# Kernel tuning notes

Measured on AMD Instinct MI355X. Metric: run time of the kernel, lower is better.

The kernel has to match this reference:

```python
import jax, jax.numpy as jnp
import numpy as np

L, B, F, D = 12, 2048, 6144, 768

def setup_inputs() -> dict:
    key = jax.random.key(0)
    k1, k2, k3 = jax.random.split(key, 3)
    acts = jax.random.normal(k1, (L, B, F), dtype=jnp.float32)
    # decoder weights for target layer: stacked per source layer, [L, F, D]
    W = jax.random.normal(k2, (L, F, D), dtype=jnp.float32) * 0.02
    bias = jax.random.normal(k3, (L, D), dtype=jnp.float32) * 0.01
    return {"acts": acts, "W": W, "bias": bias, "layer_idx": 11}

def reference(acts, W, bias, layer_idx):
    # decode(): sum over src_layer <= layer_idx of Linear(a[src], W[src->tgt], b[src->tgt])
    n = layer_idx + 1  # static Python int -> static slice
    a = acts[:n]       # [n, B, F]
    w = W[:n]          # [n, F, D]
    b = bias[:n]       # [n, D]
    # fused accumulation of all per-source-layer GEMMs
    recon = jnp.einsum('lbf,lfd->bd', a, w) + jnp.sum(b, axis=0)  # [B, D]
    return recon
```

## Files before the change

kernel.cpp:

```cpp
#include <hip/hip_runtime.h>
#include <hip/hip_bf16.h>

#define NB 2048
#define NF 6144
#define ND 768
#define BM 256
#define BN 192
#define BK 64
#define SPLITK 2
#define KCH (NF / SPLITK)
#define NTIL (KCH / BK)

#define ABYTES (BM * 128)
#define BBYTES (BN * 128)
#define BUFBYTES (ABYTES + BBYTES)

typedef __attribute__((ext_vector_type(8))) __bf16 bf16x8;
typedef __attribute__((ext_vector_type(4))) float f32x4;

__device__ __forceinline__ char* lds_addr(char* base, int row, int k) {
  const int blk = ((k >> 3) ^ (row & 7) ^ ((row >> 2) & 7)) & 7;
  return base + row * 128 + (blk << 4) + ((k & 7) << 1);
}

#define SBAR0() __builtin_amdgcn_sched_barrier(0)
#define LGKM0()                                            \
  do {                                                     \
    asm volatile("s_waitcnt lgkmcnt(0)" ::: "memory");     \
    SBAR0();                                               \
  } while (0)

__global__ __launch_bounds__(256) void bias_init_kernel(
    const float* __restrict__ bias, const int* __restrict__ lidx,
    float* __restrict__ out) {
  int n = lidx[0] + 1;
  int i = blockIdx.x * 256 + threadIdx.x;
  if (i >= NB * ND) return;
  int d = i % ND;
  float s = 0.f;
  for (int l = 0; l < n; ++l) s += bias[l * ND + d];
  out[i] = s;
}

__global__ __launch_bounds__(512, 2) void gemm_kernel(
    const float* __restrict__ acts, const float* __restrict__ W,
    const int* __restrict__ lidx, float* __restrict__ out, int nwg) {
  extern __shared__ char cbuf[];

  const int chunk = nwg >> 3;
  const int swz = (blockIdx.x & 7) * chunk + (blockIdx.x >> 3);
  const int by = swz & 3;
  int rem = swz >> 2;
  const int m = rem & 7; rem >>= 3;
  const int ks = rem & 1; rem >>= 1;
  const int l = rem;
  if (l > lidx[0]) return;

  const int brow = m * BM;
  const int ncol = by * BN;
  const int k0 = ks * KCH;

  const int tid = threadIdx.x;
  const int lane = tid & 63;
  const int wid = tid >> 6;
  const int wrow = (wid >> 1) * 64;
  const int wcol = (wid & 1) * 96;

  f32x4 acc[4][6];
#pragma unroll
  for (int i = 0; i < 4; ++i)
#pragma unroll
    for (int j = 0; j < 6; ++j) acc[i][j] = (f32x4){0.f, 0.f, 0.f, 0.f};

  const int s_arow = tid >> 3;
  const int s_ak = (tid & 7) * 8;
  const bool bstage = tid < 384;
  const int s_bd = (tid % 48) * 4;
  const int s_bk = (tid / 48) * 8;

  const float* Aptr =
      acts + (size_t)l * NB * NF + (size_t)(brow + s_arow) * NF + k0 + s_ak;
  const float* Bptr =
      W + (size_t)l * NF * ND + (size_t)(k0 + s_bk) * ND + (ncol + s_bd);

  float4 av[4][2];
  float4 bv[8];

  auto LOADS = [&](int kb) {
#pragma unroll
    for (int p = 0; p < 4; ++p) {
      av[p][0] = *(const float4*)(Aptr + (size_t)(64 * p) * NF + kb);
      av[p][1] = *(const float4*)(Aptr + (size_t)(64 * p) * NF + kb + 4);
    }
    if (bstage) {
#pragma unroll
      for (int j = 0; j < 8; ++j)
        bv[j] = *(const float4*)(Bptr + (size_t)(kb + j) * ND);
    }
  };

  auto STORE = [&](char* cA_, char* cB_) {
#pragma unroll
    for (int p = 0; p < 4; ++p) {
      bf16x8 h;
      h[0] = (__bf16)av[p][0].x; h[1] = (__bf16)av[p][0].y;
      h[2] = (__bf16)av[p][0].z; h[3] = (__bf16)av[p][0].w;
      h[4] = (__bf16)av[p][1].x; h[5] = (__bf16)av[p][1].y;
      h[6] = (__bf16)av[p][1].z; h[7] = (__bf16)av[p][1].w;
      *(bf16x8*)lds_addr(cA_, s_arow + 64 * p, s_ak) = h;
    }
    if (bstage) {
#pragma unroll
      for (int dd = 0; dd < 4; ++dd) {
        bf16x8 h;
#pragma unroll
        for (int j = 0; j < 8; ++j) h[j] = (__bf16)bv[j][dd];
        *(bf16x8*)lds_addr(cB_, s_bd + dd, s_bk) = h;
      }
    }
  };

  LOADS(0);
  STORE(cbuf, cbuf + ABYTES);

  for (int t = 0; t < NTIL; ++t) {
    const int cur = t & 1;
    char* rA = cbuf + (size_t)cur * BUFBYTES;
    char* rB = rA + ABYTES;
    char* wA = cbuf + (size_t)(cur ^ 1) * BUFBYTES;
    char* wB = wA + ABYTES;

    LGKM0();
    __builtin_amdgcn_s_barrier();
    SBAR0();

    if (t + 1 < NTIL) LOADS((t + 1) * BK);
    SBAR0();

    bf16x8 aF[4][2];
#pragma unroll
    for (int mi = 0; mi < 4; ++mi)
#pragma unroll
      for (int s = 0; s < 2; ++s)
        aF[mi][s] = *(const bf16x8*)lds_addr(
            rA, wrow + mi * 16 + (lane & 15), s * 32 + (lane >> 4) * 8);

#pragma unroll
    for (int p = 0; p < 3; ++p) {
      bf16x8 bF[2][2];
#pragma unroll
      for (int ni = 0; ni < 2; ++ni)
#pragma unroll
        for (int s = 0; s < 2; ++s)
          bF[ni][s] = *(const bf16x8*)lds_addr(
              rB, wcol + (2 * p + ni) * 16 + (lane & 15),
              s * 32 + (lane >> 4) * 8);
      LGKM0();
      __builtin_amdgcn_s_setprio(1);
#pragma unroll
      for (int s = 0; s < 2; ++s)
#pragma unroll
        for (int mi = 0; mi < 4; ++mi)
#pragma unroll
          for (int ni = 0; ni < 2; ++ni)
            acc[mi][2 * p + ni] = __builtin_amdgcn_mfma_f32_16x16x32_bf16(
                aF[mi][s], bF[ni][s], acc[mi][2 * p + ni], 0, 0, 0);
      __builtin_amdgcn_s_setprio(0);
      SBAR0();
    }

    if (t + 1 < NTIL) STORE(wA, wB);
  }

  const int orow = brow + wrow + ((lane >> 4) << 2);
  const int ocol = ncol + wcol + (lane & 15);
#pragma unroll
  for (int mi = 0; mi < 4; ++mi)
#pragma unroll
    for (int ni = 0; ni < 6; ++ni)
#pragma unroll
      for (int j = 0; j < 4; ++j)
        atomicAdd(out + (size_t)(orow + mi * 16 + j) * ND + (ocol + ni * 16),
                  acc[mi][ni][j]);
}

extern "C" void kernel_launch(void* const* d_in, const int* in_sizes, int n_in,
                              void* d_out, int out_size, void* d_ws, size_t ws_size,
                              hipStream_t stream) {
  const float* acts = (const float*)d_in[0];
  const float* W    = (const float*)d_in[1];
  const float* bias = (const float*)d_in[2];
  const int*   lidx = (const int*)d_in[3];
  float* out = (float*)d_out;

  const int L = in_sizes[0] / (NB * NF);
  const int nwg = (ND / BN) * (NB / BM) * SPLITK * L;

  hipFuncSetAttribute((const void*)gemm_kernel,
                      hipFuncAttributeMaxDynamicSharedMemorySize, 2 * BUFBYTES);

  bias_init_kernel<<<dim3((NB * ND + 255) / 256), 256, 0, stream>>>(bias, lidx, out);
  gemm_kernel<<<dim3(nwg), 512, 2 * BUFBYTES, stream>>>(acts, W, lidx, out, nwg);
}
```

Baseline: 475.8 us.

## Use 12 waves per block and split K-tile into two staged phases

Raises the workgroup from 8 to 12 waves, with each wave computing a 64x64 sub-tile instead of 64x96, so register pressure drops and more waves can hide latency. The BK=64 tile is processed in two 32-wide phases. The global loads and the bf16 LDS stores of the A tile are split across these phases so memory traffic interleaves with MFMA work. Staging is rebalanced so 512 threads load A and all 768 threads load B with 4-row chunks. The risks are more barrier participants, more LDS store instructions, and possible occupancy limits from launch_bounds(768,3) given the LDS footprint.

```diff
diff --git a/kernel.cpp b/kernel.cpp
--- a/kernel.cpp
+++ b/kernel.cpp
@@ -15,6 +15,7 @@
 #define BBYTES (BN * 128)
 #define BUFBYTES (ABYTES + BBYTES)
 
+typedef __attribute__((ext_vector_type(4))) __bf16 bf16x4;
 typedef __attribute__((ext_vector_type(8))) __bf16 bf16x8;
 typedef __attribute__((ext_vector_type(4))) float f32x4;
 
@@ -42,7 +43,7 @@
   out[i] = s;
 }
 
-__global__ __launch_bounds__(512, 2) void gemm_kernel(
+__global__ __launch_bounds__(768, 3) void gemm_kernel(
     const float* __restrict__ acts, const float* __restrict__ W,
     const int* __restrict__ lidx, float* __restrict__ out, int nwg) {
   extern __shared__ char cbuf[];
@@ -63,65 +64,109 @@
   const int tid = threadIdx.x;
   const int lane = tid & 63;
   const int wid = tid >> 6;
-  const int wrow = (wid >> 1) * 64;
-  const int wcol = (wid & 1) * 96;
-
-  f32x4 acc[4][6];
+  const int wrow = (wid / 3) * 64;
+  const int wcol = (wid % 3) * 64;
+
+  f32x4 acc[4][4];
 #pragma unroll
   for (int i = 0; i < 4; ++i)
 #pragma unroll
-    for (int j = 0; j < 6; ++j) acc[i][j] = (f32x4){0.f, 0.f, 0.f, 0.f};
-
+    for (int j = 0; j < 4; ++j) acc[i][j] = (f32x4){0.f, 0.f, 0.f, 0.f};
+
+  const bool astage = tid < 512;
   const int s_arow = tid >> 3;
   const int s_ak = (tid & 7) * 8;
-  const bool bstage = tid < 384;
-  const int s_bd = (tid % 48) * 4;
-  const int s_bk = (tid / 48) * 8;
-
   const float* Aptr =
       acts + (size_t)l * NB * NF + (size_t)(brow + s_arow) * NF + k0 + s_ak;
+  float4 av0[2][2], av1[2][2];
+
+  const int s_bd = (tid % 48) * 4;
+  const int s_bk = (tid / 48) * 4;
   const float* Bptr =
       W + (size_t)l * NF * ND + (size_t)(k0 + s_bk) * ND + (ncol + s_bd);
-
-  float4 av[4][2];
-  float4 bv[8];
-
-  auto LOADS = [&](int kb) {
-#pragma unroll
-    for (int p = 0; p < 4; ++p) {
-      av[p][0] = *(const float4*)(Aptr + (size_t)(64 * p) * NF + kb);
-      av[p][1] = *(const float4*)(Aptr + (size_t)(64 * p) * NF + kb + 4);
-    }
-    if (bstage) {
-#pragma unroll
-      for (int j = 0; j < 8; ++j)
-        bv[j] = *(const float4*)(Bptr + (size_t)(kb + j) * ND);
-    }
-  };
-
-  auto STORE = [&](char* cA_, char* cB_) {
-#pragma unroll
-    for (int p = 0; p < 4; ++p) {
-      bf16x8 h;
-      h[0] = (__bf16)av[p][0].x; h[1] = (__bf16)av[p][0].y;
-      h[2] = (__bf16)av[p][0].z; h[3] = (__bf16)av[p][0].w;
-      h[4] = (__bf16)av[p][1].x; h[5] = (__bf16)av[p][1].y;
-      h[6] = (__bf16)av[p][1].z; h[7] = (__bf16)av[p][1].w;
-      *(bf16x8*)lds_addr(cA_, s_arow + 64 * p, s_ak) = h;
-    }
-    if (bstage) {
-#pragma unroll
-      for (int dd = 0; dd < 4; ++dd) {
-        bf16x8 h;
-#pragma unroll
-        for (int j = 0; j < 8; ++j) h[j] = (__bf16)bv[j][dd];
-        *(bf16x8*)lds_addr(cB_, s_bd + dd, s_bk) = h;
-      }
-    }
-  };
-
-  LOADS(0);
-  STORE(cbuf, cbuf + ABYTES);
+  float4 bv[4];
+
+#define ALOADS0(kb)                                                          \
+  do {                                                                       \
+    if (astage) {                                                            \
+      _Pragma("unroll") for (int p = 0; p < 2; ++p) {                        \
+        av0[p][0] = *(const float4*)(Aptr + (size_t)(64 * p) * NF + (kb));   \
+        av0[p][1] = *(const float4*)(Aptr + (size_t)(64 * p) * NF + (kb) + 4); \
+      }                                                                      \
+    }                                                                        \
+  } while (0)
+#define ALOADS1(kb)                                                          \
+  do {                                                                       \
+    if (astage) {                                                            \
+      _Pragma("unroll") for (int p = 0; p < 2; ++p) {                        \
+        av1[p][0] = *(const float4*)(Aptr + (size_t)(64 * (2 + p)) * NF + (kb)); \
+        av1[p][1] = *(const float4*)(Aptr + (size_t)(64 * (2 + p)) * NF + (kb) + 4); \
+      }                                                                      \
+    }                                                                        \
+  } while (0)
+#define ASTORE0(cA_)                                                         \
+  do {                                                                       \
+    if (astage) {                                                            \
+      _Pragma("unroll") for (int p = 0; p < 2; ++p) {                        \
+        bf16x8 h;                                                            \
+        h[0] = (__bf16)av0[p][0].x; h[1] = (__bf16)av0[p][0].y;              \
+        h[2] = (__bf16)av0[p][0].z; h[3] = (__bf16)av0[p][0].w;              \
+        h[4] = (__bf16)av0[p][1].x; h[5] = (__bf16)av0[p][1].y;              \
+        h[6] = (__bf16)av0[p][1].z; h[7] = (__bf16)av0[p][1].w;              \
+        *(bf16x8*)lds_addr((cA_), s_arow + 64 * p, s_ak) = h;                \
+      }                                                                      \
+    }                                                                        \
+  } while (0)
+#define ASTORE1(cA_)                                                         \
+  do {                                                                       \
+    if (astage) {                                                            \
+      _Pragma("unroll") for (int p = 0; p < 2; ++p) {                        \
+        bf16x8 h;                                                            \
+        h[0] = (__bf16)av1[p][0].x; h[1] = (__bf16)av1[p][0].y;              \
+        h[2] = (__bf16)av1[p][0].z; h[3] = (__bf16)av1[p][0].w;              \
+        h[4] = (__bf16)av1[p][1].x; h[5] = (__bf16)av1[p][1].y;              \
+        h[6] = (__bf16)av1[p][1].z; h[7] = (__bf16)av1[p][1].w;              \
+        *(bf16x8*)lds_addr((cA_), s_arow + 64 * (2 + p), s_ak) = h;          \
+      }                                                                      \
+    }                                                                        \
+  } while (0)
+#define BLOADS(kb)                                                           \
+  do {                                                                       \
+    _Pragma("unroll") for (int j = 0; j < 4; ++j)                            \
+      bv[j] = *(const float4*)(Bptr + (size_t)((kb) + j) * ND);              \
+  } while (0)
+#define BSTORE(cB_)                                                          \
+  do {                                                                       \
+    _Pragma("unroll") for (int dd = 0; dd < 4; ++dd) {                       \
+      bf16x4 h;                                                              \
+      h[0] = (__bf16)bv[0][dd]; h[1] = (__bf16)bv[1][dd];                    \
+      h[2] = (__bf16)bv[2][dd]; h[3] = (__bf16)bv[3][dd];                    \
+      *(bf16x4*)lds_addr((cB_), s_bd + dd, s_bk) = h;                        \
+    }                                                                        \
+  } while (0)
+
+#define PHASE(S)                                                             \
+  do {                                                                       \
+    bf16x8 aF[4], bF[4];                                                     \
+    _Pragma("unroll") for (int mi = 0; mi < 4; ++mi)                         \
+      aF[mi] = *(const bf16x8*)lds_addr(                                     \
+          rA, wrow + mi * 16 + (lane & 15), (S) * 32 + (lane >> 4) * 8);     \
+    _Pragma("unroll") for (int ni = 0; ni < 4; ++ni)                         \
+      bF[ni] = *(const bf16x8*)lds_addr(                                     \
+          rB, wcol + ni * 16 + (lane & 15), (S) * 32 + (lane >> 4) * 8);     \
+    LGKM0();                                                                 \
+    __builtin_amdgcn_s_setprio(1);                                           \
+    _Pragma("unroll") for (int mi = 0; mi < 4; ++mi)                         \
+      _Pragma("unroll") for (int ni = 0; ni < 4; ++ni)                       \
+        acc[mi][ni] = __builtin_amdgcn_mfma_f32_16x16x32_bf16(               \
+            aF[mi], bF[ni], acc[mi][ni], 0, 0, 0);                           \
+    __builtin_amdgcn_s_setprio(0);                                           \
+    SBAR0();                                                                 \
+  } while (0)
+
+  ALOADS0(0); ASTORE0(cbuf);
+  ALOADS1(0); ASTORE1(cbuf);
+  BLOADS(0);  BSTORE(cbuf + ABYTES);
 
   for (int t = 0; t < NTIL; ++t) {
     const int cur = t & 1;
@@ -129,55 +174,37 @@
     char* rB = rA + ABYTES;
     char* wA = cbuf + (size_t)(cur ^ 1) * BUFBYTES;
     char* wB = wA + ABYTES;
+    const bool more = (t + 1 < NTIL);
 
     LGKM0();
     __builtin_amdgcn_s_barrier();
     SBAR0();
 
-    if (t + 1 < NTIL) LOADS((t + 1) * BK);
+    if (more) { ALOADS0((t + 1) * BK); BLOADS((t + 1) * BK); }
     SBAR0();
-
-    bf16x8 aF[4][2];
-#pragma unroll
-    for (int mi = 0; mi < 4; ++mi)
-#pragma unroll
-      for (int s = 0; s < 2; ++s)
-        aF[mi][s] = *(const bf16x8*)lds_addr(
-            rA, wrow + mi * 16 + (lane & 15), s * 32 + (lane >> 4) * 8);
-
-#pragma unroll
-    for (int p = 0; p < 3; ++p) {
-      bf16x8 bF[2][2];
-#pragma unroll
-      for (int ni = 0; ni < 2; ++ni)
-#pragma unroll
-        for (int s = 0; s < 2; ++s)
-          bF[ni][s] = *(const bf16x8*)lds_addr(
-              rB, wcol + (2 * p + ni) * 16 + (lane & 15),
-              s * 32 + (lane >> 4) * 8);
-      LGKM0();
-      __builtin_amdgcn_s_setprio(1);
-#pragma unroll
-      for (int s = 0; s < 2; ++s)
-#pragma unroll
-        for (int mi = 0; mi < 4; ++mi)
-#pragma unroll
-          for (int ni = 0; ni < 2; ++ni)
-            acc[mi][2 * p + ni] = __builtin_amdgcn_mfma_f32_16x16x32_bf16(
-                aF[mi][s], bF[ni][s], acc[mi][2 * p + ni], 0, 0, 0);
-      __builtin_amdgcn_s_setprio(0);
-      SBAR0();
-    }
-
-    if (t + 1 < NTIL) STORE(wA, wB);
+    PHASE(0);
+
+    if (more) { ALOADS1((t + 1) * BK); ASTORE0(wA); }
+    SBAR0();
+    PHASE(1);
+
+    if (more) { ASTORE1(wA); BSTORE(wB); }
   }
+
+#undef PHASE
+#undef ALOADS0
+#undef ALOADS1
+#undef ASTORE0
+#undef ASTORE1
+#undef BLOADS
+#undef BSTORE
 
   const int orow = brow + wrow + ((lane >> 4) << 2);
   const int ocol = ncol + wcol + (lane & 15);
 #pragma unroll
   for (int mi = 0; mi < 4; ++mi)
 #pragma unroll
-    for (int ni = 0; ni < 6; ++ni)
+    for (int ni = 0; ni < 4; ++ni)
 #pragma unroll
       for (int j = 0; j < 4; ++j)
         atomicAdd(out + (size_t)(orow + mi * 16 + j) * ND + (ocol + ni * 16),
@@ -200,5 +227,5 @@
                       hipFuncAttributeMaxDynamicSharedMemorySize, 2 * BUFBYTES);
 
   bias_init_kernel<<<dim3((NB * ND + 255) / 256), 256, 0, stream>>>(bias, lidx, out);
-  gemm_kernel<<<dim3(nwg), 512, 2 * BUFBYTES, stream>>>(acts, W, lidx, out, nwg);
-}
+  gemm_kernel<<<dim3(nwg), 768, 2 * BUFBYTES, stream>>>(acts, W, lidx, out, nwg);
+}
```

Measured after the change: 961.1 us. 102% more time.
